# Optimization experiments

Measured on AMD Instinct MI355X. Metric: run time of the kernel, lower is better.

The kernel has to match this reference:

```python
import jax, jax.numpy as jnp
import numpy as np

N, E, F, H, C1 = 50000, 1_600_000, 48, 1, 16  # nodes, edges, in_feats, heads, conv out


def setup_inputs() -> dict:
    key = jax.random.key(0)
    ks = jax.random.split(key, 12)
    in_ = jax.random.normal(ks[0], (N, F), dtype=jnp.float32)
    edge_index = jax.random.randint(ks[1], (2, E), 0, N, dtype=jnp.int64)
    labels = jax.random.bernoulli(ks[2], 0.5, (N, 1)).astype(jnp.float32)
    weights = jax.random.uniform(ks[3], (N, 1), dtype=jnp.float32) + 0.5
    s = 0.1  # PyG FeaStConv init: normal(0, 0.1)
    W = jax.random.normal(ks[4], (F, H * C1), dtype=jnp.float32) * s
    u = jax.random.normal(ks[5], (F, H), dtype=jnp.float32) * s
    c = jax.random.normal(ks[6], (H,), dtype=jnp.float32) * s
    bias = jax.random.normal(ks[7], (C1,), dtype=jnp.float32) * s
    lin1_w = jax.random.normal(ks[8], (C1, 8), dtype=jnp.float32) * (1.0 / np.sqrt(C1))
    lin1_b = jnp.zeros((8,), dtype=jnp.float32)
    out_w = jax.random.normal(ks[9], (8, 1), dtype=jnp.float32) * (1.0 / np.sqrt(8))
    out_b = jnp.zeros((1,), dtype=jnp.float32)
    return {"in_": in_, "edge_index": edge_index, "labels": labels,
            "weights": weights, "W": W, "u": u, "c": c, "bias": bias,
            "lin1_w": lin1_w, "lin1_b": lin1_b, "out_w": out_w, "out_b": out_b}


def feast_conv(x, edge_index, W, u, c, bias):
    n = x.shape[0]
    loop = jnp.arange(n, dtype=edge_index.dtype)  # add_self_loops=True
    src = jnp.concatenate([edge_index[0], loop])
    dst = jnp.concatenate([edge_index[1], loop])
    xj = x[src]                                   # [E+N, F] gather
    xi = x[dst]
    q = jax.nn.softmax((xj - xi) @ u + c, axis=-1)            # [E+N, H]
    xw = (xj @ W).reshape(-1, H, C1)                           # [E+N, H, C1]
    msg = jnp.einsum('ehc,eh->ec', xw, q)                      # [E+N, C1]
    agg = jax.ops.segment_sum(msg, dst, num_segments=n)        # scatter-sum
    deg = jax.ops.segment_sum(jnp.ones_like(dst, dtype=x.dtype), dst, num_segments=n)
    return agg / jnp.maximum(deg, 1.0)[:, None] + bias         # mean aggregation


def reference(in_, edge_index, labels, weights, W, u, c, bias, lin1_w, lin1_b, out_w, out_b):
    x = jax.nn.relu(feast_conv(in_, edge_index, W, u, c, bias))
    x = jax.nn.relu(x @ lin1_w + lin1_b)
    p = jax.nn.sigmoid(x @ out_w + out_b)                      # [N, 1]
    eps = 1e-7
    pc = jnp.clip(p, eps, 1.0 - eps)
    bce = -(labels * jnp.log(pc) + (1.0 - labels) * jnp.log(1.0 - pc))
    loss = jnp.mean(weights * bce)
    return (loss, p)
```

## Files before the change

### kernel.cpp

```cpp
#include <hip/hip_runtime.h>

constexpr int N_NODES  = 50000;
constexpr int N_EDGES  = 1600000;
constexpr int F_IN     = 48;
constexpr int C1_OUT   = 16;

constexpr int BNODES    = 64;
constexpr int NBINS     = 782;
constexpr int FILL_BLKS = 256;
constexpr int EPB       = N_EDGES / FILL_BLKS;
constexpr int SCAP      = 16;
constexpr int OCAP      = 8192;
constexpr int BIN_INTS  = FILL_BLKS * SCAP;
constexpr int LCAP      = 2600;
constexpr int XW_BLKS   = 49;

constexpr size_t OCNT_OFF  = 0;
constexpr size_t OFLOW_OFF = 256;
constexpr size_t PART_OFF  = OFLOW_OFF + (size_t)OCAP * 4;
constexpr size_t XW_OFF    = PART_OFF + 4096;
constexpr size_t CNT_OFF   = XW_OFF + (size_t)N_NODES * C1_OUT * 4;
constexpr size_t GSLOT_OFF = CNT_OFF + (size_t)NBINS * FILL_BLKS;

__device__ __forceinline__ void xw_body(int n, const float* __restrict__ x,
                                        const float* __restrict__ W,
                                        float* __restrict__ xw)
{
    const float4* xr = (const float4*)(x + (long)n * F_IN);
    float h[C1_OUT];
    #pragma unroll
    for (int c = 0; c < C1_OUT; ++c) h[c] = 0.f;
    #pragma unroll
    for (int k = 0; k < F_IN / 4; ++k) {
        float4 v = xr[k];
        #pragma unroll
        for (int c = 0; c < C1_OUT; ++c) {
            h[c] = fmaf(v.x, W[(4*k+0)*C1_OUT + c],
                   fmaf(v.y, W[(4*k+1)*C1_OUT + c],
                   fmaf(v.z, W[(4*k+2)*C1_OUT + c],
                   fmaf(v.w, W[(4*k+3)*C1_OUT + c], h[c]))));
        }
    }
    float4* o = (float4*)(xw + (long)n * C1_OUT);
    o[0] = make_float4(h[0],  h[1],  h[2],  h[3]);
    o[1] = make_float4(h[4],  h[5],  h[6],  h[7]);
    o[2] = make_float4(h[8],  h[9],  h[10], h[11]);
    o[3] = make_float4(h[12], h[13], h[14], h[15]);
}

__global__ __launch_bounds__(1024)
void k_fill_xw(const int* __restrict__ src, const int* __restrict__ dst,
               int* __restrict__ gslot, unsigned char* __restrict__ cnt2d,
               int* __restrict__ ocnt, unsigned int* __restrict__ oflow,
               const float* __restrict__ x, const float* __restrict__ W,
               float* __restrict__ xw)
{
    __shared__ int lcnt[NBINS];

    if (blockIdx.x >= FILL_BLKS) {
        int n = (blockIdx.x - FILL_BLKS) * 1024 + threadIdx.x;
        if (n < N_NODES) xw_body(n, x, W, xw);
        return;
    }

    int tid = threadIdx.x;
    if (tid < NBINS) lcnt[tid] = 0;
    __syncthreads();

    int e0 = blockIdx.x * EPB;
    for (int i = tid; i < EPB; i += 1024) {
        int e = e0 + i;
        int s = src[e], d = dst[e];
        int b = d >> 6;
        int p = atomicAdd(&lcnt[b], 1);
        if (p < SCAP) {
            gslot[((size_t)b * FILL_BLKS + blockIdx.x) * SCAP + p] = (s << 6) | (d & 63);
        } else {
            int g = atomicAdd(ocnt, 1);
            if (g < OCAP) oflow[g] = ((unsigned)s << 16) | (unsigned)d;
        }
    }
    __syncthreads();
    for (int b = tid; b < NBINS; b += 1024) {
        int c = lcnt[b];
        cnt2d[(size_t)b * FILL_BLKS + blockIdx.x] =
            (unsigned char)((c < SCAP) ? c : SCAP);
    }
}

__device__ __forceinline__ float node_epilogue(
    float4 a, int n, float inv, const float* __restrict__ xw,
    const float* __restrict__ bias, const float* __restrict__ lin1_w,
    const float* __restrict__ lin1_b, const float* __restrict__ out_w,
    const float* __restrict__ out_b, const float* __restrict__ labels,
    const float* __restrict__ weights, float* __restrict__ out,
    float* s16, int lane)
{
    if (lane < 4) {
        float4 v  = ((const float4*)(xw + (size_t)n * C1_OUT))[lane];
        float4 b4 = ((const float4*)bias)[lane];
        float4 h;
        h.x = fmaxf(fmaf(a.x + v.x, inv, b4.x), 0.f);
        h.y = fmaxf(fmaf(a.y + v.y, inv, b4.y), 0.f);
        h.z = fmaxf(fmaf(a.z + v.z, inv, b4.z), 0.f);
        h.w = fmaxf(fmaf(a.w + v.w, inv, b4.w), 0.f);
        ((float4*)s16)[lane] = h;
    }
    float x2 = 0.f;
    if (lane < 8) {
        x2 = lin1_b[lane];
        #pragma unroll
        for (int k = 0; k < C1_OUT; ++k)
            x2 = fmaf(s16[k], lin1_w[k * 8 + lane], x2);
        x2 = fmaxf(x2, 0.f) * out_w[lane];
    }
    x2 += __shfl_xor(x2, 1, 64);
    x2 += __shfl_xor(x2, 2, 64);
    x2 += __shfl_xor(x2, 4, 64);
    float ret = 0.f;
    if (lane == 0) {
        float z = x2 + out_b[0];
        float p = 1.f / (1.f + __expf(-z));
        out[1 + n] = p;
        const float eps = 1e-7f;
        float pc = fminf(fmaxf(p, eps), 1.f - eps);
        float y  = labels[n];
        ret = weights[n] * (-(y * __logf(pc) + (1.f - y) * __logf(1.f - pc)));
    }
    return ret;
}

__global__ __launch_bounds__(256)
void k_agg(const int* __restrict__ gslot, const unsigned char* __restrict__ cnt2d,
           const int* __restrict__ ocnt, const unsigned int* __restrict__ oflow,
           const float* __restrict__ xw,
           const float* __restrict__ bias, const float* __restrict__ lin1_w,
           const float* __restrict__ lin1_b, const float* __restrict__ out_w,
           const float* __restrict__ out_b, const float* __restrict__ labels,
           const float* __restrict__ weights, float* __restrict__ out,
           float* __restrict__ partials)
{
    __shared__ int   hist[BNODES];
    __shared__ int   cursor[BNODES];
    __shared__ int   scnt[FILL_BLKS];
    __shared__ unsigned short lbuk[LCAP];
    __shared__ float s16[4][16];
    __shared__ float sLossW[4];

    int B = blockIdx.x, tid = threadIdx.x, lane = tid & 63, w = tid >> 6;

    if (tid < BNODES) hist[tid] = 0;
    scnt[tid] = cnt2d[(size_t)B * FILL_BLKS + tid];
    __syncthreads();

    const int4* sp = (const int4*)(gslot + (size_t)B * BIN_INTS);
    int4 q0 = sp[tid], q1 = sp[tid + 256], q2 = sp[tid + 512], q3 = sp[tid + 768];
    int r0 = scnt[(tid)          >> 2] - ((tid & 3) << 2);
    int r1 = scnt[(tid + 256)    >> 2] - ((tid & 3) << 2);
    int r2 = scnt[(tid + 512)    >> 2] - ((tid & 3) << 2);
    int r3 = scnt[(tid + 768)    >> 2] - ((tid & 3) << 2);

    int oc = *ocnt; if (oc > OCAP) oc = OCAP;

    #define H4(q, r) { if (0 < (r)) atomicAdd(&hist[(q).x & 63], 1); \
                       if (1 < (r)) atomicAdd(&hist[(q).y & 63], 1); \
                       if (2 < (r)) atomicAdd(&hist[(q).z & 63], 1); \
                       if (3 < (r)) atomicAdd(&hist[(q).w & 63], 1); }
    H4(q0, r0); H4(q1, r1); H4(q2, r2); H4(q3, r3);
    #undef H4
    for (int i = tid; i < oc; i += 256) {
        int d = (int)(oflow[i] & 0xffffu);
        if ((d >> 6) == B) atomicAdd(&hist[d & 63], 1);
    }
    __syncthreads();

    if (tid < 64) {
        int val = hist[tid];
        int s = val;
        #pragma unroll
        for (int off = 1; off < 64; off <<= 1) {
            int u = __shfl_up(s, off, 64);
            if (lane >= off) s += u;
        }
        cursor[tid] = s - val;
    }
    __syncthreads();

    #define SC1(v) { int p = atomicAdd(&cursor[(v) & 63], 1); \
                     if (p < LCAP) lbuk[p] = (unsigned short)((unsigned)(v) >> 6); }
    #define SC4(q, r) { if (0 < (r)) SC1((q).x); if (1 < (r)) SC1((q).y); \
                        if (2 < (r)) SC1((q).z); if (3 < (r)) SC1((q).w); }
    SC4(q0, r0); SC4(q1, r1); SC4(q2, r2); SC4(q3, r3);
    #undef SC4
    for (int i = tid; i < oc; i += 256) {
        unsigned v = oflow[i];
        int d = (int)(v & 0xffffu);
        if ((d >> 6) == B) {
            int p = atomicAdd(&cursor[d & 63], 1);
            if (p < LCAP) lbuk[p] = (unsigned short)(v >> 16);
        }
    }
    #undef SC1
    __syncthreads();

    int rslot = lane >> 2, c4 = lane & 3;
    float lossw = 0.f;
    for (int i = 0; i < 16; ++i) {
        int ln = w * 16 + i;
        int n = B * BNODES + ln;
        if (n >= N_NODES) break;
        int deg   = hist[ln];
        int start = cursor[ln] - deg;
        float4 a = make_float4(0.f, 0.f, 0.f, 0.f);
        for (int j0 = 0; j0 < deg; j0 += 16) {
            int j = j0 + rslot;
            if (j < deg && start + j < LCAP) {
                int s = lbuk[start + j];
                float4 v = ((const float4*)(xw + (size_t)s * C1_OUT))[c4];
                a.x += v.x; a.y += v.y; a.z += v.z; a.w += v.w;
            }
        }
        #pragma unroll
        for (int off = 4; off < 64; off <<= 1) {
            a.x += __shfl_xor(a.x, off, 64);
            a.y += __shfl_xor(a.y, off, 64);
            a.z += __shfl_xor(a.z, off, 64);
            a.w += __shfl_xor(a.w, off, 64);
        }
        lossw += node_epilogue(a, n, 1.f / (float)(deg + 1), xw, bias, lin1_w,
                               lin1_b, out_w, out_b, labels, weights, out,
                               s16[w], lane);
    }
    if (lane == 0) sLossW[w] = lossw;
    __syncthreads();
    if (tid == 0)
        partials[B] = sLossW[0] + sLossW[1] + sLossW[2] + sLossW[3];
}

__global__ __launch_bounds__(1024)
void k_loss_final(const float* __restrict__ partials, float* __restrict__ out)
{
    __shared__ float sw[16];
    int tid = threadIdx.x, lane = tid & 63, wv = tid >> 6;
    float s = (tid < NBINS) ? partials[tid] : 0.f;
    #pragma unroll
    for (int off = 32; off > 0; off >>= 1) s += __shfl_down(s, off, 64);
    if (lane == 0) sw[wv] = s;
    __syncthreads();
    if (tid == 0) {
        float t = 0.f;
        #pragma unroll
        for (int k = 0; k < 16; ++k) t += sw[k];
        out[0] = t / (float)N_NODES;
    }
}

extern "C" void kernel_launch(void* const* d_in, const int* in_sizes, int n_in,
                              void* d_out, int out_size, void* d_ws, size_t ws_size,
                              hipStream_t stream)
{
    const float* x       = (const float*)d_in[0];
    const int*   eidx    = (const int*)  d_in[1];
    const float* labels  = (const float*)d_in[2];
    const float* weights = (const float*)d_in[3];
    const float* W       = (const float*)d_in[4];
    const float* bias    = (const float*)d_in[7];
    const float* lin1_w  = (const float*)d_in[8];
    const float* lin1_b  = (const float*)d_in[9];
    const float* out_w   = (const float*)d_in[10];
    const float* out_b   = (const float*)d_in[11];
    float* out = (float*)d_out;

    const int* src = eidx;
    const int* dst = eidx + N_EDGES;
    char* ws = (char*)d_ws;

    int*           ocnt     = (int*)(ws + OCNT_OFF);
    unsigned int*  oflow    = (unsigned int*)(ws + OFLOW_OFF);
    float*         partials = (float*)(ws + PART_OFF);
    float*         xw       = (float*)(ws + XW_OFF);
    unsigned char* cnt2d    = (unsigned char*)(ws + CNT_OFF);
    int*           gslot    = (int*)(ws + GSLOT_OFF);

    hipMemsetAsync(ocnt, 0, sizeof(int), stream);
    k_fill_xw<<<FILL_BLKS + XW_BLKS, 1024, 0, stream>>>(
        src, dst, gslot, cnt2d, ocnt, oflow, x, W, xw);
    k_agg<<<NBINS, 256, 0, stream>>>(
        gslot, cnt2d, ocnt, oflow, xw, bias, lin1_w, lin1_b,
        out_w, out_b, labels, weights, out, partials);
    k_loss_final<<<1, 1024, 0, stream>>>(partials, out);
}
```

Measured before the change: 158.2 us.

## Stage edge slots in LDS, pad with sentinels, and bucket per-node rows directly

```diff
diff --git a/kernel.cpp b/kernel.cpp
--- a/kernel.cpp
+++ b/kernel.cpp
@@ -10,17 +10,16 @@
 constexpr int FILL_BLKS = 256;
 constexpr int EPB       = N_EDGES / FILL_BLKS;
 constexpr int SCAP      = 16;
-constexpr int OCAP      = 8192;
+constexpr int OCAP      = 16384;
 constexpr int BIN_INTS  = FILL_BLKS * SCAP;
-constexpr int LCAP      = 2600;
+constexpr int ROWCAP    = 96;
 constexpr int XW_BLKS   = 49;
 
 constexpr size_t OCNT_OFF  = 0;
 constexpr size_t OFLOW_OFF = 256;
 constexpr size_t PART_OFF  = OFLOW_OFF + (size_t)OCAP * 4;
 constexpr size_t XW_OFF    = PART_OFF + 4096;
-constexpr size_t CNT_OFF   = XW_OFF + (size_t)N_NODES * C1_OUT * 4;
-constexpr size_t GSLOT_OFF = CNT_OFF + (size_t)NBINS * FILL_BLKS;
+constexpr size_t GSLOT_OFF = XW_OFF + (size_t)N_NODES * C1_OUT * 4;
 
 __device__ __forceinline__ void xw_body(int n, const float* __restrict__ x,
                                         const float* __restrict__ W,
@@ -50,12 +49,13 @@
 
 __global__ __launch_bounds__(1024)
 void k_fill_xw(const int* __restrict__ src, const int* __restrict__ dst,
-               int* __restrict__ gslot, unsigned char* __restrict__ cnt2d,
-               int* __restrict__ ocnt, unsigned int* __restrict__ oflow,
+               int* __restrict__ gslot, int* __restrict__ ocnt,
+               unsigned int* __restrict__ oflow,
                const float* __restrict__ x, const float* __restrict__ W,
                float* __restrict__ xw)
 {
     __shared__ int lcnt[NBINS];
+    __shared__ int lstage[NBINS * SCAP];
 
     if (blockIdx.x >= FILL_BLKS) {
         int n = (blockIdx.x - FILL_BLKS) * 1024 + threadIdx.x;
@@ -74,17 +74,18 @@
         int b = d >> 6;
         int p = atomicAdd(&lcnt[b], 1);
         if (p < SCAP) {
-            gslot[((size_t)b * FILL_BLKS + blockIdx.x) * SCAP + p] = (s << 6) | (d & 63);
+            lstage[(b << 4) + p] = (s << 6) | (d & 63);
         } else {
             int g = atomicAdd(ocnt, 1);
             if (g < OCAP) oflow[g] = ((unsigned)s << 16) | (unsigned)d;
         }
     }
     __syncthreads();
-    for (int b = tid; b < NBINS; b += 1024) {
-        int c = lcnt[b];
-        cnt2d[(size_t)b * FILL_BLKS + blockIdx.x] =
-            (unsigned char)((c < SCAP) ? c : SCAP);
+
+    for (int idx = tid; idx < NBINS * SCAP; idx += 1024) {
+        int b = idx >> 4, s = idx & 15;
+        int v = (s < lcnt[b]) ? lstage[idx] : -1;
+        gslot[((size_t)b * FILL_BLKS + blockIdx.x) * SCAP + s] = v;
     }
 }
 
@@ -131,76 +132,44 @@
 }
 
 __global__ __launch_bounds__(256)
-void k_agg(const int* __restrict__ gslot, const unsigned char* __restrict__ cnt2d,
-           const int* __restrict__ ocnt, const unsigned int* __restrict__ oflow,
-           const float* __restrict__ xw,
+void k_agg(const int* __restrict__ gslot, const int* __restrict__ ocnt,
+           const unsigned int* __restrict__ oflow, const float* __restrict__ xw,
            const float* __restrict__ bias, const float* __restrict__ lin1_w,
            const float* __restrict__ lin1_b, const float* __restrict__ out_w,
            const float* __restrict__ out_b, const float* __restrict__ labels,
            const float* __restrict__ weights, float* __restrict__ out,
            float* __restrict__ partials)
 {
-    __shared__ int   hist[BNODES];
-    __shared__ int   cursor[BNODES];
-    __shared__ int   scnt[FILL_BLKS];
-    __shared__ unsigned short lbuk[LCAP];
+    __shared__ int ndeg[BNODES];
+    __shared__ unsigned short lrow[BNODES][ROWCAP];
     __shared__ float s16[4][16];
     __shared__ float sLossW[4];
 
     int B = blockIdx.x, tid = threadIdx.x, lane = tid & 63, w = tid >> 6;
 
-    if (tid < BNODES) hist[tid] = 0;
-    scnt[tid] = cnt2d[(size_t)B * FILL_BLKS + tid];
+    if (tid < BNODES) ndeg[tid] = 0;
     __syncthreads();
 
     const int4* sp = (const int4*)(gslot + (size_t)B * BIN_INTS);
-    int4 q0 = sp[tid], q1 = sp[tid + 256], q2 = sp[tid + 512], q3 = sp[tid + 768];
-    int r0 = scnt[(tid)          >> 2] - ((tid & 3) << 2);
-    int r1 = scnt[(tid + 256)    >> 2] - ((tid & 3) << 2);
-    int r2 = scnt[(tid + 512)    >> 2] - ((tid & 3) << 2);
-    int r3 = scnt[(tid + 768)    >> 2] - ((tid & 3) << 2);
-
+    #pragma unroll
+    for (int k = 0; k < 4; ++k) {
+        int4 q = sp[tid + (k << 8)];
+        #define SC1(v) if ((v) >= 0) { int ln = (v) & 63;               \
+            int p = atomicAdd(&ndeg[ln], 1);                            \
+            if (p < ROWCAP) lrow[ln][p] = (unsigned short)((unsigned)(v) >> 6); }
+        SC1(q.x); SC1(q.y); SC1(q.z); SC1(q.w);
+        #undef SC1
+    }
     int oc = *ocnt; if (oc > OCAP) oc = OCAP;
-
-    #define H4(q, r) { if (0 < (r)) atomicAdd(&hist[(q).x & 63], 1); \
-                       if (1 < (r)) atomicAdd(&hist[(q).y & 63], 1); \
-                       if (2 < (r)) atomicAdd(&hist[(q).z & 63], 1); \
-                       if (3 < (r)) atomicAdd(&hist[(q).w & 63], 1); }
-    H4(q0, r0); H4(q1, r1); H4(q2, r2); H4(q3, r3);
-    #undef H4
-    for (int i = tid; i < oc; i += 256) {
-        int d = (int)(oflow[i] & 0xffffu);
-        if ((d >> 6) == B) atomicAdd(&hist[d & 63], 1);
-    }
-    __syncthreads();
-
-    if (tid < 64) {
-        int val = hist[tid];
-        int s = val;
-        #pragma unroll
-        for (int off = 1; off < 64; off <<= 1) {
-            int u = __shfl_up(s, off, 64);
-            if (lane >= off) s += u;
-        }
-        cursor[tid] = s - val;
-    }
-    __syncthreads();
-
-    #define SC1(v) { int p = atomicAdd(&cursor[(v) & 63], 1); \
-                     if (p < LCAP) lbuk[p] = (unsigned short)((unsigned)(v) >> 6); }
-    #define SC4(q, r) { if (0 < (r)) SC1((q).x); if (1 < (r)) SC1((q).y); \
-                        if (2 < (r)) SC1((q).z); if (3 < (r)) SC1((q).w); }
-    SC4(q0, r0); SC4(q1, r1); SC4(q2, r2); SC4(q3, r3);
-    #undef SC4
     for (int i = tid; i < oc; i += 256) {
         unsigned v = oflow[i];
         int d = (int)(v & 0xffffu);
         if ((d >> 6) == B) {
-            int p = atomicAdd(&cursor[d & 63], 1);
-            if (p < LCAP) lbuk[p] = (unsigned short)(v >> 16);
-        }
-    }
-    #undef SC1
+            int ln = d & 63;
+            int p = atomicAdd(&ndeg[ln], 1);
+            if (p < ROWCAP) lrow[ln][p] = (unsigned short)(v >> 16);
+        }
+    }
     __syncthreads();
 
     int rslot = lane >> 2, c4 = lane & 3;
@@ -209,13 +178,13 @@
         int ln = w * 16 + i;
         int n = B * BNODES + ln;
         if (n >= N_NODES) break;
-        int deg   = hist[ln];
-        int start = cursor[ln] - deg;
+        int deg = ndeg[ln];
+        if (deg > ROWCAP) deg = ROWCAP;
         float4 a = make_float4(0.f, 0.f, 0.f, 0.f);
         for (int j0 = 0; j0 < deg; j0 += 16) {
             int j = j0 + rslot;
-            if (j < deg && start + j < LCAP) {
-                int s = lbuk[start + j];
+            if (j < deg) {
+                int s = lrow[ln][j];
                 float4 v = ((const float4*)(xw + (size_t)s * C1_OUT))[c4];
                 a.x += v.x; a.y += v.y; a.z += v.z; a.w += v.w;
             }
@@ -275,18 +244,17 @@
     const int* dst = eidx + N_EDGES;
     char* ws = (char*)d_ws;
 
-    int*           ocnt     = (int*)(ws + OCNT_OFF);
-    unsigned int*  oflow    = (unsigned int*)(ws + OFLOW_OFF);
-    float*         partials = (float*)(ws + PART_OFF);
-    float*         xw       = (float*)(ws + XW_OFF);
-    unsigned char* cnt2d    = (unsigned char*)(ws + CNT_OFF);
-    int*           gslot    = (int*)(ws + GSLOT_OFF);
+    int*          ocnt     = (int*)(ws + OCNT_OFF);
+    unsigned int* oflow    = (unsigned int*)(ws + OFLOW_OFF);
+    float*        partials = (float*)(ws + PART_OFF);
+    float*        xw       = (float*)(ws + XW_OFF);
+    int*          gslot    = (int*)(ws + GSLOT_OFF);
 
     hipMemsetAsync(ocnt, 0, sizeof(int), stream);
     k_fill_xw<<<FILL_BLKS + XW_BLKS, 1024, 0, stream>>>(
-        src, dst, gslot, cnt2d, ocnt, oflow, x, W, xw);
+        src, dst, gslot, ocnt, oflow, x, W, xw);
     k_agg<<<NBINS, 256, 0, stream>>>(
-        gslot, cnt2d, ocnt, oflow, xw, bias, lin1_w, lin1_b,
+        gslot, ocnt, oflow, xw, bias, lin1_w, lin1_b,
         out_w, out_b, labels, weights, out, partials);
     k_loss_final<<<1, 1024, 0, stream>>>(partials, out);
 }
```

Result: slower. 168.0 us (+6.2%).
